# Kernel tuning notes

Hardware: AMD Instinct MI355X
Metric: run time of the kernel (lower is better)

Reference implementation:

```python
import jax, jax.numpy as jnp
import numpy as np

NUM_ENT, SEQ, H, OUT, NG = 10000, 10, 200, 100, 2048


def _seg_mean(x, idx, n):
    s = jax.ops.segment_sum(x, idx, num_segments=n)
    d = jax.ops.segment_sum(jnp.ones((idx.shape[0],), x.dtype), idx, num_segments=n)
    return s / jnp.maximum(d, 1.0)[:, None]


def setup_inputs() -> dict:
    k = jax.random.split(jax.random.key(0), 24)
    N, E, Nw, Ew, Vw, Rsel, MQ = 50000, 200000, 30000, 300000, 40000, 8192, 8
    f = lambda i, shp: jax.random.normal(k[i], shp, jnp.float32) * 0.05
    ri = lambda i, shp, hi: jax.random.randint(k[i], shp, 0, hi)
    return dict(
        ent_embeds=f(0, (NUM_ENT, H)), rel_embeds=f(1, (240, H)), word_embeds=f(2, (Vw, OUT)),
        gcn_w1=f(3, (OUT, H)), gcn_b1=jnp.zeros((H,), jnp.float32),
        gcn_w2=f(4, (H, H)), gcn_b2=jnp.zeros((H,), jnp.float32),
        cg1_wn=f(5, (H, OUT)), cg1_wl=f(6, (H, OUT)), cg1_wr=f(7, (H, OUT)),
        cg2_wn=f(8, (OUT, H)), cg2_wl=f(9, (OUT, H)), cg2_wr=f(10, (OUT, H)),
        attn_wa=f(11, (H, H)), attn_wc=f(12, (2 * H, H)),
        node_slot=jnp.arange(N), edge_src=ri(13, (E,), N), edge_dst=ri(14, (E,), N),
        edge_type=ri(15, (E,), 240), word_id=ri(16, (Nw,), Vw),
        wsrc=ri(17, (Ew,), Nw), wdst=ri(18, (Ew,), Nw),
        ent_word_idx=ri(19, (N, MQ), Nw), ent_word_mask=ri(20, (N, MQ), 2).astype(jnp.int32),
        rel_word_idx=ri(21, (Rsel, MQ), Nw), rel_word_mask=ri(22, (Rsel, MQ), 2).astype(jnp.int32),
        r_ids_graph=ri(23, (Rsel,), E), edge_slot=jnp.arange(Rsel))


def reference(ent_embeds, rel_embeds, word_embeds, gcn_w1, gcn_b1, gcn_w2, gcn_b2,
              cg1_wn, cg1_wl, cg1_wr, cg2_wn, cg2_wl, cg2_wr, attn_wa, attn_wc,
              node_slot, edge_src, edge_dst, edge_type, word_id, wsrc, wdst,
              ent_word_idx, ent_word_mask, rel_word_idx, rel_word_mask, r_ids_graph, edge_slot):
    N = node_slot.shape[0]
    Nw = word_id.shape[0]
    Rsel = r_ids_graph.shape[0]
    # --- se_aggr: 2-layer GCN over the batched word graph ---
    wh = word_embeds[word_id]                                   # [Nw,100]
    wh = jax.nn.relu(_seg_mean(wh[wsrc], wdst, Nw) @ gcn_w1 + gcn_b1)
    wh = jax.nn.relu(_seg_mean(wh[wsrc], wdst, Nw) @ gcn_w2 + gcn_b2)
    # --- re_aggr1/re_aggr2: CompGCN message passing on batched event graph ---
    h = ent_embeds[node_slot % NUM_ENT]                         # [N,200]
    e = rel_embeds[edge_type]                                   # [E,200]
    def compgcn(h, e, wn, wl, wr):
        agg = _seg_mean(h[edge_src] - e, edge_dst, N)           # sub-composition msgs
        return jax.nn.relu(agg @ wn + h @ wl), e @ wr
    h, e = compgcn(h, e, cg1_wn, cg1_wl, cg1_wr)                # 200 -> 100
    h, e = compgcn(h, e, cg2_wn, cg2_wl, cg2_wr)                # 100 -> 200
    embeds_g_r = e[r_ids_graph]                                 # [Rsel,200]
    # --- build Q_mx / H_mx (padded word-context groups) + 'general' attention ---
    Q = jnp.concatenate([h, embeds_g_r], 0)                     # [N+Rsel,200]
    H_ent = wh[ent_word_idx] * ent_word_mask[..., None].astype(wh.dtype)   # [N,8,200]
    H_rel = wh[rel_word_idx] * rel_word_mask[..., None].astype(wh.dtype)   # [Rsel,8,200]
    Hm = jnp.concatenate([H_ent, H_rel], 0)                     # [N+Rsel,8,200]
    scores = jnp.einsum('md,de,mke->mk', Q, attn_wa, Hm)
    attn = jax.nn.softmax(scores, axis=-1)
    ctx = jnp.einsum('mk,mkd->md', attn, Hm)
    out = jnp.tanh(jnp.concatenate([ctx, Q], -1) @ attn_wc)     # [N+Rsel,200]
    h_out, r_out = out[:N], out[N:]
    # --- temporal scatter of node embeddings per snapshot graph ---
    nid = node_slot % NUM_ENT
    gidx = node_slot // (N // SEQ)
    node_emb_temporal = jnp.zeros((NUM_ENT, SEQ, H), h_out.dtype).at[nid, gidx].set(h_out)
    # --- pack selected edge embeds into padded [NG, SEQ, H] sequence tensor ---
    per = Rsel // NG
    row, pos = edge_slot // per, edge_slot % per
    embed_seq = jnp.zeros((NG, SEQ, H), r_out.dtype).at[row, pos].set(r_out)
    return embed_seq, node_emb_temporal
```

## Files before the change

### kernel.cpp

```cpp
#include <hip/hip_runtime.h>
#include <cstddef>

constexpr int NUM_ENT_C = 10000;
constexpr int SEQ_C     = 10;
constexpr int H_C       = 200;
constexpr int OUT_C     = 100;
constexpr int NG_C      = 2048;
constexpr int NREL_C    = 240;
constexpr int MQ_C      = 8;

typedef __attribute__((ext_vector_type(8))) short          bf16x8;
typedef __attribute__((ext_vector_type(4))) float          f32x4;
typedef __attribute__((ext_vector_type(8))) unsigned short u16x8;

__device__ __forceinline__ unsigned short f2bf(float v) {
    unsigned u = __float_as_uint(v);
    unsigned r = (u + 0x7FFFu + ((u >> 16) & 1u)) >> 16;
    return (unsigned short)r;
}

__global__ void hist_k(const int* __restrict__ dIdx, int* __restrict__ deg, int E) {
    int stride = gridDim.x * blockDim.x;
    for (int t = blockIdx.x * blockDim.x + threadIdx.x; t < E; t += stride)
        atomicAdd(&deg[dIdx[t]], 1);
}

__global__ void scanA_k(const int* __restrict__ v, int* __restrict__ bsum, int n) {
    __shared__ int s[256];
    int t = threadIdx.x;
    int i = blockIdx.x * 256 + t;
    s[t] = (i < n) ? v[i] : 0;
    __syncthreads();
    for (int d = 128; d; d >>= 1) {
        if (t < d) s[t] += s[t + d];
        __syncthreads();
    }
    if (t == 0) bsum[blockIdx.x] = s[0];
}

__global__ void scanB_k(int* __restrict__ bsum, int nb) {
    __shared__ int s[256];
    int t = threadIdx.x;
    int v = (t < nb) ? bsum[t] : 0;
    s[t] = v;
    __syncthreads();
    for (int d = 1; d < 256; d <<= 1) {
        int x = (t >= d) ? s[t - d] : 0;
        __syncthreads();
        s[t] += x;
        __syncthreads();
    }
    if (t < nb) bsum[t] = s[t] - v;
}

__global__ void scanC_k(const int* __restrict__ v, const int* __restrict__ bsum,
                        int* __restrict__ offs, int* __restrict__ cur, int n) {
    __shared__ int s[256];
    int t = threadIdx.x;
    int i = blockIdx.x * 256 + t;
    int val = (i < n) ? v[i] : 0;
    s[t] = val;
    __syncthreads();
    for (int d = 1; d < 256; d <<= 1) {
        int x = (t >= d) ? s[t - d] : 0;
        __syncthreads();
        s[t] += x;
        __syncthreads();
    }
    if (i < n) {
        int ex = s[t] - val + bsum[blockIdx.x];
        offs[i] = ex;
        cur[i]  = ex;
    }
}

__global__ void fill_k(const int* __restrict__ dIdx, int* __restrict__ cur,
                       int* __restrict__ bkt, int E) {
    int stride = gridDim.x * blockDim.x;
    for (int t = blockIdx.x * blockDim.x + threadIdx.x; t < E; t += stride) {
        int d = dIdx[t];
        int p = atomicAdd(&cur[d], 1);
        bkt[p] = t;
    }
}

template<int K1, int K2, int Kp, int SRCMODE, bool RELSUB, bool SELFMOD>
__global__ __launch_bounds__(256) void gather_mean_k(
        const float* __restrict__ feat, const float* __restrict__ selfFeat,
        const float* __restrict__ rel,
        const int* __restrict__ srcIdx, const int* __restrict__ typeIdx,
        const int* __restrict__ wordId,
        const int* __restrict__ offs, const int* __restrict__ deg,
        const int* __restrict__ bkt,
        unsigned short* __restrict__ dst, int n) {
    constexpr int NCH = (Kp + 63) / 64;
    int node = blockIdx.x * 4 + (threadIdx.x >> 6);
    int lane = threadIdx.x & 63;
    if (node >= n) return;
    float acc[NCH];
    #pragma unroll
    for (int c = 0; c < NCH; ++c) acc[c] = 0.f;
    int off = offs[node], dg = deg[node];
    for (int i = 0; i < dg; ++i) {
        int e = bkt[off + i];
        int s = srcIdx[e];
        if (SRCMODE == 1) s = wordId[s];
        if (SRCMODE == 2) s = s % NUM_ENT_C;
        const float* fr = feat + (size_t)s * K1;
        const float* rr = RELSUB ? rel + (size_t)typeIdx[e] * K1 : nullptr;
        #pragma unroll
        for (int c = 0; c < NCH; ++c) {
            int col = c * 64 + lane;
            if (col < K1) {
                float v = fr[col];
                if (RELSUB) v -= rr[col];
                acc[c] += v;
            }
        }
    }
    float inv = 1.f / fmaxf((float)dg, 1.f);
    int srow = SELFMOD ? (node % NUM_ENT_C) : node;
    unsigned short* drow = dst + (size_t)node * Kp;
    #pragma unroll
    for (int c = 0; c < NCH; ++c) {
        int col = c * 64 + lane;
        if (col >= Kp) continue;
        float v;
        if (col < K1)            v = acc[c] * inv;
        else if (col < K1 + K2)  v = selfFeat[(size_t)srow * K2 + (col - K1)];
        else                     v = 0.f;
        drow[col] = f2bf(v);
    }
}

__global__ void convW_k(const float* __restrict__ W1, int K1,
                        const float* __restrict__ W2, int K2, int N,
                        unsigned short* __restrict__ dst, int Nt, int Kp) {
    int total  = Nt * Kp;
    int stride = gridDim.x * blockDim.x;
    for (int t = blockIdx.x * blockDim.x + threadIdx.x; t < total; t += stride) {
        int n = t / Kp;
        int k = t - n * Kp;
        float v = 0.0f;
        if (n < N) {
            if (k < K1)           v = W1[(size_t)k * N + n];
            else if (k < K1 + K2) v = W2[(size_t)(k - K1) * N + n];
        }
        dst[t] = f2bf(v);
    }
}

__global__ void build_q_bf16_k(const float* __restrict__ rel2, const int* __restrict__ edge_type,
                               const int* __restrict__ r_ids, unsigned short* __restrict__ A,
                               int N, int M) {
    int R = M - N;
    size_t total  = (size_t)R * H_C;
    size_t stride = (size_t)gridDim.x * blockDim.x;
    for (size_t t = (size_t)blockIdx.x * blockDim.x + threadIdx.x; t < total; t += stride) {
        int r = (int)(t / H_C);
        int d = (int)(t - (size_t)r * H_C);
        int rr = r_ids[r];
        A[(size_t)(N + r) * 448 + 200 + d] = f2bf(rel2[(size_t)edge_type[rr] * H_C + d]);
    }
}

__global__ void zero_pad_k(unsigned short* __restrict__ A, int M) {
    int total  = M * 6;
    int stride = gridDim.x * blockDim.x;
    for (int t = blockIdx.x * blockDim.x + threadIdx.x; t < total; t += stride) {
        int m = t / 6, c = t - m * 6;
        *reinterpret_cast<uint4*>(A + (size_t)m * 448 + 400 + c * 8) = make_uint4(0u, 0u, 0u, 0u);
    }
}

__global__ void rowoff_k(const int* __restrict__ node_slot, const int* __restrict__ edge_slot,
                         int* __restrict__ rowOff, int N, int M, int divq, int per, int embBase) {
    int stride = gridDim.x * blockDim.x;
    for (int m = blockIdx.x * blockDim.x + threadIdx.x; m < M; m += stride) {
        int off;
        if (m < N) {
            int ns = node_slot[m];
            int nid  = ns % NUM_ENT_C;
            int gidx = ns / divq;
            off = embBase + (nid * SEQ_C + gidx) * H_C;
        } else {
            int es  = edge_slot[m - N];
            int row = es / per;
            int pos = es - row * per;
            off = (row * SEQ_C + pos) * H_C;
        }
        rowOff[m] = off;
    }
}

template<int NF, int ACT, bool SCATTER, bool OBF16>
__global__ __launch_bounds__(256) void mfma_gemm_k(
        const unsigned short* __restrict__ A, int lda,
        const unsigned short* __restrict__ Wt,
        const float* __restrict__ bias, void* __restrict__ Cv, int ldc,
        const int* __restrict__ rowOff, int M, int N, int Kp) {
    constexpr int BN = NF * 16;
    __shared__ unsigned short As[64][40];
    __shared__ unsigned short Bs[BN][40];
    const int tid  = threadIdx.x;
    const int bm   = blockIdx.x * 64;
    const int w    = tid >> 6;
    const int lane = tid & 63;
    const int lr   = lane & 15;
    const int lk   = (lane >> 4) * 8;

    f32x4 acc[NF];
    #pragma unroll
    for (int nf = 0; nf < NF; ++nf) acc[nf] = (f32x4){0.f, 0.f, 0.f, 0.f};

    for (int k0 = 0; k0 < Kp; k0 += 32) {
        {
            int m = tid >> 2, c = tid & 3;
            int gm = bm + m;
            uint4 v = make_uint4(0u, 0u, 0u, 0u);
            if (gm < M) v = *reinterpret_cast<const uint4*>(A + (size_t)gm * lda + k0 + c * 8);
            *reinterpret_cast<uint4*>(&As[m][c * 8]) = v;
        }
        for (int i = tid; i < NF * 64; i += 256) {
            int n = i >> 2, c = i & 3;
            uint4 v = *reinterpret_cast<const uint4*>(Wt + (size_t)n * Kp + k0 + c * 8);
            *reinterpret_cast<uint4*>(&Bs[n][c * 8]) = v;
        }
        __syncthreads();
        bf16x8 a = *reinterpret_cast<const bf16x8*>(&As[w * 16 + lr][lk]);
        #pragma unroll
        for (int nf = 0; nf < NF; ++nf) {
            bf16x8 b = *reinterpret_cast<const bf16x8*>(&Bs[nf * 16 + lr][lk]);
            acc[nf] = __builtin_amdgcn_mfma_f32_16x16x32_bf16(a, b, acc[nf], 0, 0, 0);
        }
        __syncthreads();
    }

    const int r0 = (lane >> 4) * 4;
    #pragma unroll
    for (int j = 0; j < 4; ++j) {
        int gm = bm + w * 16 + r0 + j;
        if (gm >= M) continue;
        size_t base;
        if (OBF16)        base = (size_t)gm * ldc;
        else if (SCATTER) base = (size_t)rowOff[gm];
        else              base = (size_t)gm * ldc;
        #pragma unroll
        for (int nf = 0; nf < NF; ++nf) {
            int gn = nf * 16 + lr;
            if (gn >= N) continue;
            float v = acc[nf][j];
            if (bias) v += bias[gn];
            if (ACT == 1) v = fmaxf(v, 0.f);
            if (ACT == 2) v = tanhf(v);
            if (OBF16) ((unsigned short*)Cv)[base + gn] = f2bf(v);
            else       ((float*)Cv)[base + gn] = v;
        }
    }
}

template<int NF, int ACT, bool SCATTER, bool OBF16>
static void launch_mfma(hipStream_t s, const unsigned short* A, int lda,
                        const unsigned short* Wt, const float* bias,
                        void* C, int ldc, const int* rowOff, int M, int N, int Kp) {
    mfma_gemm_k<NF, ACT, SCATTER, OBF16><<<dim3((M + 63) / 64), 256, 0, s>>>(
        A, lda, Wt, bias, C, ldc, rowOff, M, N, Kp);
}

__global__ __launch_bounds__(256) void gemm_f32_k(
        const float* __restrict__ A, const float* __restrict__ W,
        float* __restrict__ C, int M, int N, int K) {
    constexpr int TS = 64, BK = 16;
    __shared__ float As[BK][TS];
    __shared__ float Bs[BK][TS];
    int bm = blockIdx.x * TS, bn = blockIdx.y * TS;
    int tid = threadIdx.x;
    int tx = tid & 15, ty = tid >> 4;
    float acc[4][4] = {};
    for (int k0 = 0; k0 < K; k0 += BK) {
        #pragma unroll
        for (int l = tid; l < TS * BK; l += 256) {
            int m = l >> 4, kk = l & 15;
            int gm = bm + m, gk = k0 + kk;
            As[kk][m] = (gm < M && gk < K) ? A[(size_t)gm * K + gk] : 0.f;
        }
        #pragma unroll
        for (int l = tid; l < TS * BK; l += 256) {
            int kk = l >> 6, n = l & 63;
            int gk = k0 + kk, gn = bn + n;
            Bs[kk][n] = (gk < K && gn < N) ? W[(size_t)gk * N + gn] : 0.f;
        }
        __syncthreads();
        #pragma unroll
        for (int kk = 0; kk < BK; ++kk) {
            float a[4], b[4];
            #pragma unroll
            for (int i = 0; i < 4; ++i) a[i] = As[kk][ty * 4 + i];
            #pragma unroll
            for (int j = 0; j < 4; ++j) b[j] = Bs[kk][tx * 4 + j];
            #pragma unroll
            for (int i = 0; i < 4; ++i)
                #pragma unroll
                for (int j = 0; j < 4; ++j) acc[i][j] += a[i] * b[j];
        }
        __syncthreads();
    }
    #pragma unroll
    for (int i = 0; i < 4; ++i) {
        int gm = bm + ty * 4 + i;
        if (gm >= M) continue;
        #pragma unroll
        for (int j = 0; j < 4; ++j) {
            int gn = bn + tx * 4 + j;
            if (gn < N) C[(size_t)gm * N + gn] = acc[i][j];
        }
    }
}

__global__ __launch_bounds__(256) void attn_k(
        const float* __restrict__ QA, const float* __restrict__ wh,
        const int* __restrict__ ent_idx, const int* __restrict__ ent_mask,
        const int* __restrict__ rel_idx, const int* __restrict__ rel_mask,
        unsigned short* __restrict__ ctxOut, int N, int M) {
    int wave = (int)(((size_t)blockIdx.x * blockDim.x + threadIdx.x) >> 6);
    int lane = threadIdx.x & 63;
    if (wave >= M) return;
    int m = wave;
    const int* idxp;
    const int* mskp;
    if (m < N) { idxp = ent_idx + (size_t)m * MQ_C;        mskp = ent_mask + (size_t)m * MQ_C; }
    else       { idxp = rel_idx + (size_t)(m - N) * MQ_C;  mskp = rel_mask + (size_t)(m - N) * MQ_C; }

    float qa[4];
    #pragma unroll
    for (int j = 0; j < 4; ++j) {
        int d = j * 64 + lane;
        qa[j] = (d < H_C) ? QA[(size_t)m * H_C + d] : 0.f;
    }
    int   idx[MQ_C];
    float msk[MQ_C];
    float s[MQ_C];
    #pragma unroll
    for (int k = 0; k < MQ_C; ++k) { idx[k] = idxp[k]; msk[k] = (float)mskp[k]; }
    #pragma unroll
    for (int k = 0; k < MQ_C; ++k) {
        const float* w = wh + (size_t)idx[k] * H_C;
        float p = 0.f;
        #pragma unroll
        for (int j = 0; j < 4; ++j) {
            int d = j * 64 + lane;
            if (d < H_C) p += qa[j] * w[d];
        }
        #pragma unroll
        for (int off = 32; off; off >>= 1) p += __shfl_xor(p, off);
        s[k] = p * msk[k];
    }
    float mx = s[0];
    #pragma unroll
    for (int k = 1; k < MQ_C; ++k) mx = fmaxf(mx, s[k]);
    float den = 0.f;
    #pragma unroll
    for (int k = 0; k < MQ_C; ++k) { s[k] = expf(s[k] - mx); den += s[k]; }
    float inv = 1.f / den;
    #pragma unroll
    for (int j = 0; j < 4; ++j) {
        int d = j * 64 + lane;
        if (d >= H_C) continue;
        float c = 0.f;
        #pragma unroll
        for (int k = 0; k < MQ_C; ++k) c += s[k] * msk[k] * wh[(size_t)idx[k] * H_C + d];
        ctxOut[(size_t)m * 448 + d] = f2bf(c * inv);
    }
}


static inline dim3 ew_grid(size_t total) {
    size_t b = (total + 255) / 256;
    if (b > 4096) b = 4096;
    return dim3((unsigned)b);
}

extern "C" void kernel_launch(void* const* d_in, const int* in_sizes, int n_in,
                              void* d_out, int out_size, void* d_ws, size_t ws_size,
                              hipStream_t stream) {
    const float* ent_embeds = (const float*)d_in[0];
    const float* rel_embeds = (const float*)d_in[1];
    const float* word_embeds= (const float*)d_in[2];
    const float* gcn_w1     = (const float*)d_in[3];
    const float* gcn_b1     = (const float*)d_in[4];
    const float* gcn_w2     = (const float*)d_in[5];
    const float* gcn_b2     = (const float*)d_in[6];
    const float* cg1_wn     = (const float*)d_in[7];
    const float* cg1_wl     = (const float*)d_in[8];
    const float* cg1_wr     = (const float*)d_in[9];
    const float* cg2_wn     = (const float*)d_in[10];
    const float* cg2_wl     = (const float*)d_in[11];
    const float* cg2_wr     = (const float*)d_in[12];
    const float* attn_wa    = (const float*)d_in[13];
    const float* attn_wc    = (const float*)d_in[14];
    const int* node_slot    = (const int*)d_in[15];
    const int* edge_src     = (const int*)d_in[16];
    const int* edge_dst     = (const int*)d_in[17];
    const int* edge_type    = (const int*)d_in[18];
    const int* word_id      = (const int*)d_in[19];
    const int* wsrc         = (const int*)d_in[20];
    const int* wdst         = (const int*)d_in[21];
    const int* ent_word_idx = (const int*)d_in[22];
    const int* ent_word_mask= (const int*)d_in[23];
    const int* rel_word_idx = (const int*)d_in[24];
    const int* rel_word_mask= (const int*)d_in[25];
    const int* r_ids_graph  = (const int*)d_in[26];
    const int* edge_slot    = (const int*)d_in[27];

    const int N    = in_sizes[15];
    const int E    = in_sizes[16];
    const int Nw   = in_sizes[19];
    const int Ew   = in_sizes[20];
    const int Rsel = in_sizes[27];
    const int M    = N + Rsel;
    const int divq = N / SEQ_C;
    const int per  = Rsel / NG_C;
    const int embBase = NG_C * SEQ_C * H_C;

    float* ws = (float*)d_ws;
    size_t o = 0;
    int* wdeg  = (int*)(ws + o); o += Nw;
    int* woffs = (int*)(ws + o); o += Nw;
    int* wcur  = (int*)(ws + o); o += Nw;
    int* edeg  = (int*)(ws + o); o += N;
    int* eoffs = (int*)(ws + o); o += N;
    int* ecur  = (int*)(ws + o); o += N;
    int* wbkt  = (int*)(ws + o); o += Ew;
    int* ebkt  = (int*)(ws + o); o += E;
    int* bsum  = (int*)(ws + o); o += 256;
    int* rowOff= (int*)(ws + o); o += M;
    float* rel1 = ws + o; o += (size_t)NREL_C * OUT_C;
    float* rel2 = ws + o; o += (size_t)NREL_C * H_C;
    o = (o + 3) & ~(size_t)3;
    unsigned short* Wt = (unsigned short*)(ws + o); o += (208 * 448) / 2;
    float* wh = ws + o; o += (size_t)Nw * H_C;
    float* h1 = ws + o; o += (size_t)N * OUT_C;
    o = (o + 3) & ~(size_t)3;
    unsigned short* AbfF = (unsigned short*)(ws + o); o += ((size_t)M * 448) / 2;
    o = (o + 3) & ~(size_t)3;
    float* BIG = ws + o;
    float* wh1 = BIG;
    unsigned short* AbfW = (unsigned short*)(BIG + (size_t)Nw * H_C);
    unsigned short* AbfE = (unsigned short*)BIG;
    float* QA = (float*)d_out;

    hipMemsetAsync(wdeg, 0, (size_t)Nw * 4, stream);
    hipMemsetAsync(edeg, 0, (size_t)N * 4, stream);
    hist_k<<<ew_grid(Ew), 256, 0, stream>>>(wdst, wdeg, Ew);
    hist_k<<<ew_grid(E), 256, 0, stream>>>(edge_dst, edeg, E);
    {
        int nbW = (Nw + 255) / 256;
        scanA_k<<<nbW, 256, 0, stream>>>(wdeg, bsum, Nw);
        scanB_k<<<1, 256, 0, stream>>>(bsum, nbW);
        scanC_k<<<nbW, 256, 0, stream>>>(wdeg, bsum, woffs, wcur, Nw);
        fill_k<<<ew_grid(Ew), 256, 0, stream>>>(wdst, wcur, wbkt, Ew);
        int nbE = (N + 255) / 256;
        scanA_k<<<nbE, 256, 0, stream>>>(edeg, bsum, N);
        scanB_k<<<1, 256, 0, stream>>>(bsum, nbE);
        scanC_k<<<nbE, 256, 0, stream>>>(edeg, bsum, eoffs, ecur, N);
        fill_k<<<ew_grid(E), 256, 0, stream>>>(edge_dst, ecur, ebkt, E);
    }
    gemm_f32_k<<<dim3((NREL_C + 63) / 64, (OUT_C + 63) / 64), 256, 0, stream>>>(
        rel_embeds, cg1_wr, rel1, NREL_C, OUT_C, H_C);
    gemm_f32_k<<<dim3((NREL_C + 63) / 64, (H_C + 63) / 64), 256, 0, stream>>>(
        rel1, cg2_wr, rel2, NREL_C, H_C, OUT_C);

    gather_mean_k<OUT_C, 0, 128, 1, false, false><<<dim3((Nw + 3) / 4), 256, 0, stream>>>(
        word_embeds, nullptr, nullptr, wsrc, nullptr, word_id, woffs, wdeg, wbkt, AbfW, Nw);
    convW_k<<<ew_grid(208 * 128), 256, 0, stream>>>(gcn_w1, OUT_C, nullptr, 0, H_C, Wt, 208, 128);
    launch_mfma<13, 1, false, false>(stream, AbfW, 128, Wt, gcn_b1, wh1, H_C, nullptr, Nw, H_C, 128);
    gather_mean_k<H_C, 0, 224, 0, false, false><<<dim3((Nw + 3) / 4), 256, 0, stream>>>(
        wh1, nullptr, nullptr, wsrc, nullptr, nullptr, woffs, wdeg, wbkt, AbfW, Nw);
    convW_k<<<ew_grid(208 * 224), 256, 0, stream>>>(gcn_w2, H_C, nullptr, 0, H_C, Wt, 208, 224);
    launch_mfma<13, 1, false, false>(stream, AbfW, 224, Wt, gcn_b2, wh, H_C, nullptr, Nw, H_C, 224);

    gather_mean_k<H_C, H_C, 416, 2, true, true><<<dim3((N + 3) / 4), 256, 0, stream>>>(
        ent_embeds, ent_embeds, rel_embeds, edge_src, edge_type, nullptr,
        eoffs, edeg, ebkt, AbfE, N);
    convW_k<<<ew_grid(112 * 416), 256, 0, stream>>>(cg1_wn, H_C, cg1_wl, H_C, OUT_C, Wt, 112, 416);
    launch_mfma<7, 1, false, false>(stream, AbfE, 416, Wt, nullptr, h1, OUT_C, nullptr, N, OUT_C, 416);
    gather_mean_k<OUT_C, OUT_C, 224, 0, true, false><<<dim3((N + 3) / 4), 256, 0, stream>>>(
        h1, h1, rel1, edge_src, edge_type, nullptr, eoffs, edeg, ebkt, AbfE, N);
    convW_k<<<ew_grid(208 * 224), 256, 0, stream>>>(cg2_wn, OUT_C, cg2_wl, OUT_C, H_C, Wt, 208, 224);
    launch_mfma<13, 1, false, true>(stream, AbfE, 224, Wt, nullptr, AbfF + 200, 448, nullptr, N, H_C, 224);

    build_q_bf16_k<<<ew_grid((size_t)Rsel * H_C), 256, 0, stream>>>(
        rel2, edge_type, r_ids_graph, AbfF, N, M);
    zero_pad_k<<<ew_grid((size_t)M * 6), 256, 0, stream>>>(AbfF, M);
    rowoff_k<<<ew_grid(M), 256, 0, stream>>>(node_slot, edge_slot, rowOff, N, M, divq, per, embBase);
    convW_k<<<ew_grid(208 * 224), 256, 0, stream>>>(attn_wa, H_C, nullptr, 0, H_C, Wt, 208, 224);
    launch_mfma<13, 0, false, false>(stream, AbfF + 200, 448, Wt, nullptr, QA, H_C, nullptr, M, H_C, 224);
    attn_k<<<(M + 3) / 4, 256, 0, stream>>>(QA, wh, ent_word_idx, ent_word_mask,
                                            rel_word_idx, rel_word_mask, AbfF, N, M);
    hipMemsetAsync(d_out, 0, (size_t)out_size * 4, stream);
    convW_k<<<ew_grid(208 * 416), 256, 0, stream>>>(attn_wc, H_C, attn_wc + (size_t)H_C * H_C,
                                                    H_C, H_C, Wt, 208, 416);
    launch_mfma<13, 2, true, false>(stream, AbfF, 448, Wt, nullptr, d_out, H_C, rowOff, M, H_C, 416);
}
```

Before: 830.5 us.

## Store intermediate features in bf16 and widen MFMA GEMM tile to 128 rows

```diff
diff --git a/kernel.cpp b/kernel.cpp
--- a/kernel.cpp
+++ b/kernel.cpp
@@ -17,6 +17,21 @@
     unsigned u = __float_as_uint(v);
     unsigned r = (u + 0x7FFFu + ((u >> 16) & 1u)) >> 16;
     return (unsigned short)r;
+}
+__device__ __forceinline__ float bf2f(unsigned short b) {
+    return __uint_as_float((unsigned)b << 16);
+}
+
+__global__ void f2bf_arr_k(const float* __restrict__ src, unsigned short* __restrict__ dst,
+                           size_t n8) {
+    size_t stride = (size_t)gridDim.x * blockDim.x;
+    for (size_t t = (size_t)blockIdx.x * blockDim.x + threadIdx.x; t < n8; t += stride) {
+        const float* s = src + t * 8;
+        u16x8 o;
+        #pragma unroll
+        for (int i = 0; i < 8; ++i) o[i] = f2bf(s[i]);
+        *reinterpret_cast<u16x8*>(dst + t * 8) = o;
+    }
 }
 
 __global__ void hist_k(const int* __restrict__ dIdx, int* __restrict__ deg, int E) {
@@ -84,9 +99,9 @@
     }
 }
 
-template<int K1, int K2, int Kp, int SRCMODE, bool RELSUB, bool SELFMOD>
+template<int K1, int K2, int Kp, int SRCMODE, bool RELSUB, bool SELFMOD, bool BF16IN>
 __global__ __launch_bounds__(256) void gather_mean_k(
-        const float* __restrict__ feat, const float* __restrict__ selfFeat,
+        const void* __restrict__ featv, const void* __restrict__ selfv,
         const float* __restrict__ rel,
         const int* __restrict__ srcIdx, const int* __restrict__ typeIdx,
         const int* __restrict__ wordId,
@@ -106,15 +121,28 @@
         int s = srcIdx[e];
         if (SRCMODE == 1) s = wordId[s];
         if (SRCMODE == 2) s = s % NUM_ENT_C;
-        const float* fr = feat + (size_t)s * K1;
         const float* rr = RELSUB ? rel + (size_t)typeIdx[e] * K1 : nullptr;
-        #pragma unroll
-        for (int c = 0; c < NCH; ++c) {
-            int col = c * 64 + lane;
-            if (col < K1) {
-                float v = fr[col];
-                if (RELSUB) v -= rr[col];
-                acc[c] += v;
+        if (BF16IN) {
+            const unsigned short* fr = (const unsigned short*)featv + (size_t)s * K1;
+            #pragma unroll
+            for (int c = 0; c < NCH; ++c) {
+                int col = c * 64 + lane;
+                if (col < K1) {
+                    float v = bf2f(fr[col]);
+                    if (RELSUB) v -= rr[col];
+                    acc[c] += v;
+                }
+            }
+        } else {
+            const float* fr = (const float*)featv + (size_t)s * K1;
+            #pragma unroll
+            for (int c = 0; c < NCH; ++c) {
+                int col = c * 64 + lane;
+                if (col < K1) {
+                    float v = fr[col];
+                    if (RELSUB) v -= rr[col];
+                    acc[c] += v;
+                }
             }
         }
     }
@@ -125,11 +153,13 @@
     for (int c = 0; c < NCH; ++c) {
         int col = c * 64 + lane;
         if (col >= Kp) continue;
-        float v;
-        if (col < K1)            v = acc[c] * inv;
-        else if (col < K1 + K2)  v = selfFeat[(size_t)srow * K2 + (col - K1)];
-        else                     v = 0.f;
-        drow[col] = f2bf(v);
+        unsigned short ov;
+        if (col < K1)           ov = f2bf(acc[c] * inv);
+        else if (col < K1 + K2) {
+            if (BF16IN) ov = ((const unsigned short*)selfv)[(size_t)srow * K2 + (col - K1)];
+            else        ov = f2bf(((const float*)selfv)[(size_t)srow * K2 + (col - K1)]);
+        } else ov = 0;
+        drow[col] = ov;
     }
 }
 
@@ -200,22 +230,27 @@
         const float* __restrict__ bias, void* __restrict__ Cv, int ldc,
         const int* __restrict__ rowOff, int M, int N, int Kp) {
     constexpr int BN = NF * 16;
-    __shared__ unsigned short As[64][40];
+    __shared__ unsigned short As[128][40];
     __shared__ unsigned short Bs[BN][40];
     const int tid  = threadIdx.x;
-    const int bm   = blockIdx.x * 64;
+    const int bm   = blockIdx.x * 128;
     const int w    = tid >> 6;
     const int lane = tid & 63;
     const int lr   = lane & 15;
     const int lk   = (lane >> 4) * 8;
 
-    f32x4 acc[NF];
-    #pragma unroll
-    for (int nf = 0; nf < NF; ++nf) acc[nf] = (f32x4){0.f, 0.f, 0.f, 0.f};
+    f32x4 acc0[NF], acc1[NF];
+    #pragma unroll
+    for (int nf = 0; nf < NF; ++nf) {
+        acc0[nf] = (f32x4){0.f, 0.f, 0.f, 0.f};
+        acc1[nf] = (f32x4){0.f, 0.f, 0.f, 0.f};
+    }
 
     for (int k0 = 0; k0 < Kp; k0 += 32) {
-        {
-            int m = tid >> 2, c = tid & 3;
+        #pragma unroll
+        for (int j = 0; j < 2; ++j) {
+            int id = tid + j * 256;
+            int m = id >> 2, c = id & 3;
             int gm = bm + m;
             uint4 v = make_uint4(0u, 0u, 0u, 0u);
             if (gm < M) v = *reinterpret_cast<const uint4*>(A + (size_t)gm * lda + k0 + c * 8);
@@ -227,34 +262,38 @@
             *reinterpret_cast<uint4*>(&Bs[n][c * 8]) = v;
         }
         __syncthreads();
-        bf16x8 a = *reinterpret_cast<const bf16x8*>(&As[w * 16 + lr][lk]);
+        bf16x8 a0 = *reinterpret_cast<const bf16x8*>(&As[w * 16 + lr][lk]);
+        bf16x8 a1 = *reinterpret_cast<const bf16x8*>(&As[64 + w * 16 + lr][lk]);
         #pragma unroll
         for (int nf = 0; nf < NF; ++nf) {
             bf16x8 b = *reinterpret_cast<const bf16x8*>(&Bs[nf * 16 + lr][lk]);
-            acc[nf] = __builtin_amdgcn_mfma_f32_16x16x32_bf16(a, b, acc[nf], 0, 0, 0);
+            acc0[nf] = __builtin_amdgcn_mfma_f32_16x16x32_bf16(a0, b, acc0[nf], 0, 0, 0);
+            acc1[nf] = __builtin_amdgcn_mfma_f32_16x16x32_bf16(a1, b, acc1[nf], 0, 0, 0);
         }
         __syncthreads();
     }
 
     const int r0 = (lane >> 4) * 4;
     #pragma unroll
-    for (int j = 0; j < 4; ++j) {
-        int gm = bm + w * 16 + r0 + j;
-        if (gm >= M) continue;
-        size_t base;
-        if (OBF16)        base = (size_t)gm * ldc;
-        else if (SCATTER) base = (size_t)rowOff[gm];
-        else              base = (size_t)gm * ldc;
-        #pragma unroll
-        for (int nf = 0; nf < NF; ++nf) {
-            int gn = nf * 16 + lr;
-            if (gn >= N) continue;
-            float v = acc[nf][j];
-            if (bias) v += bias[gn];
-            if (ACT == 1) v = fmaxf(v, 0.f);
-            if (ACT == 2) v = tanhf(v);
-            if (OBF16) ((unsigned short*)Cv)[base + gn] = f2bf(v);
-            else       ((float*)Cv)[base + gn] = v;
+    for (int h = 0; h < 2; ++h) {
+        #pragma unroll
+        for (int j = 0; j < 4; ++j) {
+            int gm = bm + h * 64 + w * 16 + r0 + j;
+            if (gm >= M) continue;
+            size_t base;
+            if (SCATTER && !OBF16) base = (size_t)rowOff[gm];
+            else                   base = (size_t)gm * ldc;
+            #pragma unroll
+            for (int nf = 0; nf < NF; ++nf) {
+                int gn = nf * 16 + lr;
+                if (gn >= N) continue;
+                float v = h ? acc1[nf][j] : acc0[nf][j];
+                if (bias) v += bias[gn];
+                if (ACT == 1) v = fmaxf(v, 0.f);
+                if (ACT == 2) v = tanhf(v);
+                if (OBF16) ((unsigned short*)Cv)[base + gn] = f2bf(v);
+                else       ((float*)Cv)[base + gn] = v;
+            }
         }
     }
 }
@@ -263,7 +302,7 @@
 static void launch_mfma(hipStream_t s, const unsigned short* A, int lda,
                         const unsigned short* Wt, const float* bias,
                         void* C, int ldc, const int* rowOff, int M, int N, int Kp) {
-    mfma_gemm_k<NF, ACT, SCATTER, OBF16><<<dim3((M + 63) / 64), 256, 0, s>>>(
+    mfma_gemm_k<NF, ACT, SCATTER, OBF16><<<dim3((M + 127) / 128), 256, 0, s>>>(
         A, lda, Wt, bias, C, ldc, rowOff, M, N, Kp);
 }
 
@@ -318,7 +357,7 @@
 }
 
 __global__ __launch_bounds__(256) void attn_k(
-        const float* __restrict__ QA, const float* __restrict__ wh,
+        const float* __restrict__ QA, const unsigned short* __restrict__ whb,
         const int* __restrict__ ent_idx, const int* __restrict__ ent_mask,
         const int* __restrict__ rel_idx, const int* __restrict__ rel_mask,
         unsigned short* __restrict__ ctxOut, int N, int M) {
@@ -331,25 +370,35 @@
     if (m < N) { idxp = ent_idx + (size_t)m * MQ_C;        mskp = ent_mask + (size_t)m * MQ_C; }
     else       { idxp = rel_idx + (size_t)(m - N) * MQ_C;  mskp = rel_mask + (size_t)(m - N) * MQ_C; }
 
-    float qa[4];
-    #pragma unroll
-    for (int j = 0; j < 4; ++j) {
-        int d = j * 64 + lane;
-        qa[j] = (d < H_C) ? QA[(size_t)m * H_C + d] : 0.f;
+    float2 qa[2];
+    #pragma unroll
+    for (int j = 0; j < 2; ++j) {
+        int d0 = j * 128 + lane * 2;
+        qa[j] = (d0 < H_C) ? *reinterpret_cast<const float2*>(QA + (size_t)m * H_C + d0)
+                           : make_float2(0.f, 0.f);
     }
     int   idx[MQ_C];
     float msk[MQ_C];
     float s[MQ_C];
+    float2 wreg[MQ_C][2];
     #pragma unroll
     for (int k = 0; k < MQ_C; ++k) { idx[k] = idxp[k]; msk[k] = (float)mskp[k]; }
     #pragma unroll
     for (int k = 0; k < MQ_C; ++k) {
-        const float* w = wh + (size_t)idx[k] * H_C;
+        const unsigned short* w = whb + (size_t)idx[k] * H_C;
         float p = 0.f;
         #pragma unroll
-        for (int j = 0; j < 4; ++j) {
-            int d = j * 64 + lane;
-            if (d < H_C) p += qa[j] * w[d];
+        for (int j = 0; j < 2; ++j) {
+            int d0 = j * 128 + lane * 2;
+            if (d0 < H_C) {
+                unsigned u = *reinterpret_cast<const unsigned*>(w + d0);
+                float lo = __uint_as_float(u << 16);
+                float hi = __uint_as_float(u & 0xFFFF0000u);
+                wreg[k][j] = make_float2(lo, hi);
+                p += qa[j].x * lo + qa[j].y * hi;
+            } else {
+                wreg[k][j] = make_float2(0.f, 0.f);
+            }
         }
         #pragma unroll
         for (int off = 32; off; off >>= 1) p += __shfl_xor(p, off);
@@ -363,13 +412,18 @@
     for (int k = 0; k < MQ_C; ++k) { s[k] = expf(s[k] - mx); den += s[k]; }
     float inv = 1.f / den;
     #pragma unroll
-    for (int j = 0; j < 4; ++j) {
-        int d = j * 64 + lane;
-        if (d >= H_C) continue;
-        float c = 0.f;
-        #pragma unroll
-        for (int k = 0; k < MQ_C; ++k) c += s[k] * msk[k] * wh[(size_t)idx[k] * H_C + d];
-        ctxOut[(size_t)m * 448 + d] = f2bf(c * inv);
+    for (int j = 0; j < 2; ++j) {
+        int d0 = j * 128 + lane * 2;
+        if (d0 >= H_C) continue;
+        float cx = 0.f, cy = 0.f;
+        #pragma unroll
+        for (int k = 0; k < MQ_C; ++k) {
+            float a = s[k] * msk[k];
+            cx += a * wreg[k][j].x;
+            cy += a * wreg[k][j].y;
+        }
+        unsigned out = (unsigned)f2bf(cx * inv) | ((unsigned)f2bf(cy * inv) << 16);
+        *reinterpret_cast<unsigned*>(ctxOut + (size_t)m * 448 + d0) = out;
     }
 }
 
@@ -421,9 +475,12 @@
     const int divq = N / SEQ_C;
     const int per  = Rsel / NG_C;
     const int embBase = NG_C * SEQ_C * H_C;
+    const size_t entElems  = (size_t)in_sizes[0];
+    const size_t wembElems = (size_t)in_sizes[2];
 
     float* ws = (float*)d_ws;
     size_t o = 0;
+    auto align4 = [&]() { o = (o + 3) & ~(size_t)3; };
     int* wdeg  = (int*)(ws + o); o += Nw;
     int* woffs = (int*)(ws + o); o += Nw;
     int* wcur  = (int*)(ws + o); o += Nw;
@@ -436,19 +493,27 @@
     int* rowOff= (int*)(ws + o); o += M;
     float* rel1 = ws + o; o += (size_t)NREL_C * OUT_C;
     float* rel2 = ws + o; o += (size_t)NREL_C * H_C;
-    o = (o + 3) & ~(size_t)3;
-    unsigned short* Wt = (unsigned short*)(ws + o); o += (208 * 448) / 2;
-    float* wh = ws + o; o += (size_t)Nw * H_C;
-    float* h1 = ws + o; o += (size_t)N * OUT_C;
-    o = (o + 3) & ~(size_t)3;
-    unsigned short* AbfF = (unsigned short*)(ws + o); o += ((size_t)M * 448) / 2;
-    o = (o + 3) & ~(size_t)3;
+    align4();
+    unsigned short* Wt      = (unsigned short*)(ws + o); o += (208 * 448) / 2;
+    align4();
+    unsigned short* wh_bf   = (unsigned short*)(ws + o); o += ((size_t)Nw * H_C) / 2;
+    align4();
+    unsigned short* h1_bf   = (unsigned short*)(ws + o); o += ((size_t)N * OUT_C) / 2;
+    align4();
+    unsigned short* ent_bf  = (unsigned short*)(ws + o); o += entElems / 2;
+    align4();
+    unsigned short* wemb_bf = (unsigned short*)(ws + o); o += wembElems / 2;
+    align4();
+    unsigned short* AbfF    = (unsigned short*)(ws + o); o += ((size_t)M * 448) / 2;
+    align4();
     float* BIG = ws + o;
-    float* wh1 = BIG;
-    unsigned short* AbfW = (unsigned short*)(BIG + (size_t)Nw * H_C);
-    unsigned short* AbfE = (unsigned short*)BIG;
+    unsigned short* wh1_bf = (unsigned short*)BIG;
+    unsigned short* AbfW   = (unsigned short*)(BIG + ((size_t)Nw * H_C) / 2);
+    unsigned short* AbfE   = (unsigned short*)BIG;
     float* QA = (float*)d_out;
 
+    f2bf_arr_k<<<ew_grid(entElems / 8), 256, 0, stream>>>(ent_embeds, ent_bf, entElems / 8);
+    f2bf_arr_k<<<ew_grid(wembElems / 8), 256, 0, stream>>>(word_embeds, wemb_bf, wembElems / 8);
     hipMemsetAsync(wdeg, 0, (size_t)Nw * 4, stream);
     hipMemsetAsync(edeg, 0, (size_t)N * 4, stream);
     hist_k<<<ew_grid(Ew), 256, 0, stream>>>(wdst, wdeg, Ew);
@@ -470,22 +535,21 @@
     gemm_f32_k<<<dim3((NREL_C + 63) / 64, (H_C + 63) / 64), 256, 0, stream>>>(
         rel1, cg2_wr, rel2, NREL_C, H_C, OUT_C);
 
-    gather_mean_k<OUT_C, 0, 128, 1, false, false><<<dim3((Nw + 3) / 4), 256, 0, stream>>>(
-        word_embeds, nullptr, nullptr, wsrc, nullptr, word_id, woffs, wdeg, wbkt, AbfW, Nw);
+    gather_mean_k<OUT_C, 0, 128, 1, false, false, true><<<dim3((Nw + 3) / 4), 256, 0, stream>>>(
+        wemb_bf, nullptr, nullptr, wsrc, nullptr, word_id, woffs, wdeg, wbkt, AbfW, Nw);
     convW_k<<<ew_grid(208 * 128), 256, 0, stream>>>(gcn_w1, OUT_C, nullptr, 0, H_C, Wt, 208, 128);
-    launch_mfma<13, 1, false, false>(stream, AbfW, 128, Wt, gcn_b1, wh1, H_C, nullptr, Nw, H_C, 128);
-    gather_mean_k<H_C, 0, 224, 0, false, false><<<dim3((Nw + 3) / 4), 256, 0, stream>>>(
-        wh1, nullptr, nullptr, wsrc, nullptr, nullptr, woffs, wdeg, wbkt, AbfW, Nw);
+    launch_mfma<13, 1, false, true>(stream, AbfW, 128, Wt, gcn_b1, wh1_bf, H_C, nullptr, Nw, H_C, 128);
+    gather_mean_k<H_C, 0, 224, 0, false, false, true><<<dim3((Nw + 3) / 4), 256, 0, stream>>>(
+        wh1_bf, nullptr, nullptr, wsrc, nullptr, nullptr, woffs, wdeg, wbkt, AbfW, Nw);
     convW_k<<<ew_grid(208 * 224), 256, 0, stream>>>(gcn_w2, H_C, nullptr, 0, H_C, Wt, 208, 224);
-    launch_mfma<13, 1, false, false>(stream, AbfW, 224, Wt, gcn_b2, wh, H_C, nullptr, Nw, H_C, 224);
-
-    gather_mean_k<H_C, H_C, 416, 2, true, true><<<dim3((N + 3) / 4), 256, 0, stream>>>(
-        ent_embeds, ent_embeds, rel_embeds, edge_src, edge_type, nullptr,
-        eoffs, edeg, ebkt, AbfE, N);
+    launch_mfma<13, 1, false, true>(stream, AbfW, 224, Wt, gcn_b2, wh_bf, H_C, nullptr, Nw, H_C, 224);
+
+    gather_mean_k<H_C, H_C, 416, 2, true, true, true><<<dim3((N + 3) / 4), 256, 0, stream>>>(
+        ent_bf, ent_bf, rel_embeds, edge_src, edge_type, nullptr, eoffs, edeg, ebkt, AbfE, N);
     convW_k<<<ew_grid(112 * 416), 256, 0, stream>>>(cg1_wn, H_C, cg1_wl, H_C, OUT_C, Wt, 112, 416);
-    launch_mfma<7, 1, false, false>(stream, AbfE, 416, Wt, nullptr, h1, OUT_C, nullptr, N, OUT_C, 416);
-    gather_mean_k<OUT_C, OUT_C, 224, 0, true, false><<<dim3((N + 3) / 4), 256, 0, stream>>>(
-        h1, h1, rel1, edge_src, edge_type, nullptr, eoffs, edeg, ebkt, AbfE, N);
+    launch_mfma<7, 1, false, true>(stream, AbfE, 416, Wt, nullptr, h1_bf, OUT_C, nullptr, N, OUT_C, 416);
+    gather_mean_k<OUT_C, OUT_C, 224, 0, true, false, true><<<dim3((N + 3) / 4), 256, 0, stream>>>(
+        h1_bf, h1_bf, rel1, edge_src, edge_type, nullptr, eoffs, edeg, ebkt, AbfE, N);
     convW_k<<<ew_grid(208 * 224), 256, 0, stream>>>(cg2_wn, OUT_C, cg2_wl, OUT_C, H_C, Wt, 208, 224);
     launch_mfma<13, 1, false, true>(stream, AbfE, 224, Wt, nullptr, AbfF + 200, 448, nullptr, N, H_C, 224);
 
@@ -495,7 +559,7 @@
     rowoff_k<<<ew_grid(M), 256, 0, stream>>>(node_slot, edge_slot, rowOff, N, M, divq, per, embBase);
     convW_k<<<ew_grid(208 * 224), 256, 0, stream>>>(attn_wa, H_C, nullptr, 0, H_C, Wt, 208, 224);
     launch_mfma<13, 0, false, false>(stream, AbfF + 200, 448, Wt, nullptr, QA, H_C, nullptr, M, H_C, 224);
-    attn_k<<<(M + 3) / 4, 256, 0, stream>>>(QA, wh, ent_word_idx, ent_word_mask,
+    attn_k<<<(M + 3) / 4, 256, 0, stream>>>(QA, wh_bf, ent_word_idx, ent_word_mask,
                                             rel_word_idx, rel_word_mask, AbfF, N, M);
     hipMemsetAsync(d_out, 0, (size_t)out_size * 4, stream);
     convW_k<<<ew_grid(208 * 416), 256, 0, stream>>>(attn_wc, H_C, attn_wc + (size_t)H_C * H_C,
```

New measurement: 854.3 us. 2.9% more time.
